# Optimization experiments

Measured on AMD Instinct MI355X. Metric: run time of the kernel, lower is better.

## Reference

```python
import jax, jax.numpy as jnp
import numpy as np

G = 320      # padded linear-hash grid extent (256 + margin for kernel offsets)
SHIFT = 16   # shift so offset coords stay non-negative


def _lin(c):
    cs = c.astype(np.int64) + SHIFT
    return (cs[:, 0] * G + cs[:, 1]) * G + cs[:, 2]


def _build_kmap(coords_in, coords_out, s):
    """Kernel map [27, N_out]: index into coords_in for each 3^3 offset (stride s), -1 if absent."""
    keys = _lin(coords_in)
    order = np.argsort(keys)
    sk = keys[order]
    offs = np.array([[i, j, k] for i in (-s, 0, s) for j in (-s, 0, s) for k in (-s, 0, s)], np.int64)
    kmap = np.full((27, coords_out.shape[0]), -1, np.int64)
    for t in range(27):
        q = _lin(coords_out + offs[t])
        pos = np.clip(np.searchsorted(sk, q), 0, sk.shape[0] - 1)
        m = sk[pos] == q
        kmap[t] = np.where(m, order[pos], -1)
    return kmap


def _downsample(coords, ns):
    return np.unique((coords // ns) * ns, axis=0)


def setup_inputs() -> dict:
    rng = np.random.default_rng(0)
    coords0 = np.unique(rng.integers(0, 256, size=(320000, 3), dtype=np.int64), axis=0)
    coords1 = _downsample(coords0, 2)
    coords2 = _downsample(coords1, 4)
    coords3 = _downsample(coords2, 8)

    km0 = _build_kmap(coords0, coords0, 1)   # conv0, ts=1
    kmd0 = _build_kmap(coords0, coords1, 1)  # down0 -> ts=2
    km1 = _build_kmap(coords1, coords1, 2)   # conv1, ts=2
    kmd1 = _build_kmap(coords1, coords2, 2)  # down1 -> ts=4
    km2 = _build_kmap(coords2, coords2, 4)   # conv2, ts=4
    kmd2 = _build_kmap(coords2, coords3, 4)  # down2 -> ts=8

    key = jax.random.key(0)
    ks = jax.random.split(key, 13)
    p = lambda k, shp: jax.random.normal(k, shp, jnp.float32) * 0.05
    return {
        "x": jax.random.normal(ks[0], (coords0.shape[0], 3), jnp.float32),
        "km0": jnp.asarray(km0), "kmd0": jnp.asarray(kmd0),
        "km1": jnp.asarray(km1), "kmd1": jnp.asarray(kmd1),
        "km2": jnp.asarray(km2), "kmd2": jnp.asarray(kmd2),
        "W0": p(ks[1], (27, 3, 64)), "b0": p(ks[2], (64,)),
        "Wd0": p(ks[3], (27, 64, 128)), "bd0": p(ks[4], (128,)),
        "W1": p(ks[5], (27, 128, 128)), "b1": p(ks[6], (128,)),
        "Wd1": p(ks[7], (27, 128, 128)), "bd1": p(ks[8], (128,)),
        "W2": p(ks[9], (27, 128, 128)), "b2": p(ks[10], (128,)),
        "Wd2": p(ks[11], (27, 128, 128)), "bd2": p(ks[12], (128,)),
    }


def _sconv(f, kmap, W, b):
    # gather-GEMM-scatter sparse conv: out[n] = b + sum_k f[kmap[k,n]] @ W[k]
    N = kmap.shape[1]
    out = jnp.zeros((N, W.shape[2]), f.dtype) + b
    for k in range(27):  # fixed small kernel loop
        idx = kmap[k]
        g = jnp.where(idx[:, None] >= 0, f[jnp.clip(idx, 0)], 0.0)
        out = out + g @ W[k]
    return out


def reference(x, km0, kmd0, km1, kmd1, km2, kmd2,
              W0, b0, Wd0, bd0, W1, b1, Wd1, bd1, W2, b2, Wd2, bd2):
    h = _sconv(x, km0, W0, b0)
    out0 = jax.nn.relu(_sconv(h, kmd0, Wd0, bd0))
    h = _sconv(out0, km1, W1, b1)
    out1 = jax.nn.relu(_sconv(h, kmd1, Wd1, bd1))
    h = _sconv(out1, km2, W2, b2)
    out2 = _sconv(h, kmd2, Wd2, bd2)  # no relu on the last output (matches torch forward)
    return (out2, out1, out0)
```

## Files before the change

### kernel.cpp

```cpp
#include <hip/hip_runtime.h>
#include <stdint.h>

typedef __bf16 bf16x8 __attribute__((ext_vector_type(8)));
typedef float f32x4 __attribute__((ext_vector_type(4)));

__device__ __forceinline__ uint32_t f2bf(float f) {
  uint32_t u = __builtin_bit_cast(uint32_t, f);
  return (u + 0x7fffu + ((u >> 16) & 1u)) >> 16;
}

__device__ __forceinline__ void gld_lds16(const void* g, void* l) {
  __builtin_amdgcn_global_load_lds(
      (const __attribute__((address_space(1))) void*)g,
      (__attribute__((address_space(3))) void*)l, 16, 0, 0);
}

__global__ void wprep_kernel(const float* __restrict__ W, uint16_t* __restrict__ Wt, int Cin) {
  int total = 27 * Cin * 128;
  for (int i = blockIdx.x * blockDim.x + threadIdx.x; i < total; i += gridDim.x * blockDim.x) {
    int k  = i / (Cin * 128);
    int r  = i - k * Cin * 128;
    int co = r / Cin;
    int ci = r - co * Cin;
    Wt[i] = (uint16_t)f2bf(W[(k * Cin + ci) * 128 + co]);
  }
}

__global__ __launch_bounds__(256) void conv0_kernel(
    const float* __restrict__ x, const int* __restrict__ km,
    const float* __restrict__ W0, const float* __restrict__ b0,
    uint16_t* __restrict__ h0, int N) {
  __shared__ float Ws[27 * 192 + 64];
  for (int i = threadIdx.x; i < 27 * 192; i += 256) Ws[i] = W0[i];
  if (threadIdx.x < 64) Ws[27 * 192 + threadIdx.x] = b0[threadIdx.x];
  __syncthreads();
  const int n = blockIdx.x * 256 + threadIdx.x;
  if (n >= N) return;

  int idx[27];
  #pragma unroll
  for (int k = 0; k < 27; ++k) idx[k] = km[(size_t)k * N + n];

  f32x4 acc[16];
  #pragma unroll
  for (int c = 0; c < 16; ++c) acc[c] = *(const f32x4*)&Ws[27 * 192 + c * 4];

  #pragma unroll
  for (int k = 0; k < 27; ++k) {
    if (idx[k] >= 0) {
      const float* xr = x + (size_t)idx[k] * 3;
      const float x0 = xr[0], x1 = xr[1], x2 = xr[2];
      const float* wk = Ws + k * 192;
      #pragma unroll
      for (int c = 0; c < 16; ++c) {
        const f32x4 w0 = *(const f32x4*)(wk + c * 4);
        const f32x4 w1 = *(const f32x4*)(wk + 64 + c * 4);
        const f32x4 w2 = *(const f32x4*)(wk + 128 + c * 4);
        acc[c] += x0 * w0 + x1 * w1 + x2 * w2;
      }
    }
  }

  uint16_t* out = h0 + (size_t)n * 64;
  #pragma unroll
  for (int g = 0; g < 8; ++g) {
    int4 v;
    v.x = (int)(f2bf(acc[g * 2][0]) | (f2bf(acc[g * 2][1]) << 16));
    v.y = (int)(f2bf(acc[g * 2][2]) | (f2bf(acc[g * 2][3]) << 16));
    v.z = (int)(f2bf(acc[g * 2 + 1][0]) | (f2bf(acc[g * 2 + 1][1]) << 16));
    v.w = (int)(f2bf(acc[g * 2 + 1][2]) | (f2bf(acc[g * 2 + 1][3]) << 16));
    *(int4*)(out + g * 8) = v;
  }
}

template <int CIN, bool OUTF32, bool RELU, bool SHADOW>
__global__ __launch_bounds__(512, 4) void sconv_pipe2_kernel(
    const uint16_t* __restrict__ fin, const int* __restrict__ kmap,
    const uint16_t* __restrict__ Wt, const float* __restrict__ bias,
    float* __restrict__ outf, uint16_t* __restrict__ outb,
    const uint16_t* __restrict__ zp, int Nout) {
  constexpr int QH = CIN / 32;
  constexpr int S = 27 * QH;
  __shared__ __align__(16) uint16_t As[2][256 * 32];
  __shared__ __align__(16) uint16_t Bs[2][128 * 32];
  __shared__ int idxs[27 * 256];

  const int t = threadIdx.x;
  const int lane = t & 63, w = t >> 6;
  const int wr = w >> 1, wc = w & 1;

  const int nwg = gridDim.x;
  int bid = blockIdx.x;
  if (nwg >= 8) {
    const int q = nwg >> 3, r = nwg & 7;
    const int xcd = bid & 7, pos = bid >> 3;
    bid = (xcd < r ? xcd * (q + 1) : r * (q + 1) + (xcd - r) * q) + pos;
  }
  const int n0 = bid * 256;

  for (int i = t; i < 27 * 256; i += 512) {
    int n = n0 + (i & 255);
    idxs[i] = (n < Nout) ? kmap[(size_t)(i >> 8) * Nout + n] : -1;
  }
  __syncthreads();

  f32x4 acc[4][4] = {};

  auto stage = [&](int ss, int nb) {
    const int k = ss / QH;
    const int q = ss % QH;
    #pragma unroll
    for (int j = 0; j < 2; ++j) {
      const int base = w * 64 + j * 512;
      const int row = (base >> 2) + (lane >> 2);
      const int sw = (lane & 3) ^ ((row >> 1) & 3);
      const int idx = idxs[k * 256 + row];
      const void* srcA = (idx >= 0)
          ? (const void*)(fin + (size_t)idx * CIN + q * 32 + sw * 8)
          : (const void*)zp;
      gld_lds16(srcA, (char*)&As[nb][0] + base * 16);
    }
    {
      const uint16_t* wk = Wt + (size_t)k * 128 * CIN + q * 32;
      const int row = t >> 2;
      const int sw = (t & 3) ^ ((row >> 1) & 3);
      gld_lds16((const void*)(wk + (size_t)row * CIN + sw * 8),
                (char*)&Bs[nb][0] + (w * 64) * 16);
    }
  };

  stage(0, 0);
  __syncthreads();

  int cur = 0;
  for (int s = 0; s < S; ++s) {
    if (s + 1 < S) stage(s + 1, cur ^ 1);
    const char* Ab = (const char*)&As[cur][0];
    const char* Bb = (const char*)&Bs[cur][0];
    bf16x8 a[4], b[4];
    const int cl = lane >> 4;
    #pragma unroll
    for (int m = 0; m < 4; ++m) {
      int row = wr * 64 + m * 16 + (lane & 15);
      a[m] = *(const bf16x8*)(Ab + row * 64 + ((cl ^ ((row >> 1) & 3)) * 16));
    }
    #pragma unroll
    for (int n = 0; n < 4; ++n) {
      int row = wc * 64 + n * 16 + (lane & 15);
      b[n] = *(const bf16x8*)(Bb + row * 64 + ((cl ^ ((row >> 1) & 3)) * 16));
    }
    #pragma unroll
    for (int m = 0; m < 4; ++m)
      #pragma unroll
      for (int n = 0; n < 4; ++n)
        acc[m][n] = __builtin_amdgcn_mfma_f32_16x16x32_bf16(a[m], b[n], acc[m][n], 0, 0, 0);
    __syncthreads();
    cur ^= 1;
  }

  #pragma unroll
  for (int m = 0; m < 4; ++m) {
    int rbase = n0 + wr * 64 + m * 16 + ((lane >> 4) << 2);
    #pragma unroll
    for (int r = 0; r < 4; ++r) {
      int gr = rbase + r;
      if (gr < Nout) {
        #pragma unroll
        for (int n = 0; n < 4; ++n) {
          int col = wc * 64 + n * 16 + (lane & 15);
          float v = acc[m][n][r] + bias[col];
          if (RELU) v = fmaxf(v, 0.f);
          if (OUTF32) outf[(size_t)gr * 128 + col] = v;
          if (SHADOW) outb[(size_t)gr * 128 + col] = (uint16_t)f2bf(v);
        }
      }
    }
  }
}

template <int CIN, bool IN_F32, bool RELU, bool WF32>
__global__ __launch_bounds__(256) void sconv_mfma_kernel(
    const void* __restrict__ fin, const int* __restrict__ kmap,
    const uint16_t* __restrict__ Wt, const float* __restrict__ bias,
    void* __restrict__ outp, int Nout) {
  constexpr int ROWB = CIN * 2;
  constexpr int CHR  = CIN / 8;
  constexpr int CPT  = (128 * CHR) / 256;
  __shared__ __align__(16) uint16_t As[128 * CIN];
  __shared__ __align__(16) uint16_t Bs[128 * CIN];
  const int t = threadIdx.x;
  const int lane = t & 63, w = t >> 6;
  const int wr = w >> 1, wc = w & 1;
  const int n0 = blockIdx.x * 128;
  f32x4 acc[4][4] = {};
  for (int k = 0; k < 27; ++k) {
    const int* __restrict__ km = kmap + (size_t)k * Nout;
    #pragma unroll
    for (int j = 0; j < CPT; ++j) {
      int c = t + j * 256;
      int row = c / CHR, c16 = c - row * CHR;
      int n = n0 + row;
      int idx = (n < Nout) ? km[n] : -1;
      int4 v = {0, 0, 0, 0};
      if (idx >= 0) {
        if (IN_F32) {
          const float* src = (const float*)fin + (size_t)idx * CIN + c16 * 8;
          float4 lo = *(const float4*)src;
          float4 hi = *(const float4*)(src + 4);
          v.x = (int)(f2bf(lo.x) | (f2bf(lo.y) << 16));
          v.y = (int)(f2bf(lo.z) | (f2bf(lo.w) << 16));
          v.z = (int)(f2bf(hi.x) | (f2bf(hi.y) << 16));
          v.w = (int)(f2bf(hi.z) | (f2bf(hi.w) << 16));
        } else {
          v = *(const int4*)((const uint16_t*)fin + (size_t)idx * CIN + c16 * 8);
        }
      }
      *(int4*)((char*)As + row * ROWB + ((c16 * 16) ^ ((row & 7) << 4))) = v;
    }
    const uint16_t* __restrict__ wkp = Wt + (size_t)k * 128 * CIN;
    #pragma unroll
    for (int j = 0; j < CPT; ++j) {
      int c = t + j * 256;
      int row = c / CHR, c16 = c - row * CHR;
      int4 v = *(const int4*)(wkp + row * CIN + c16 * 8);
      *(int4*)((char*)Bs + row * ROWB + ((c16 * 16) ^ ((row & 7) << 4))) = v;
    }
    __syncthreads();
    #pragma unroll
    for (int kk = 0; kk < CIN / 32; ++kk) {
      const int kb = (kk * 32 + ((lane >> 4) * 8)) * 2;
      bf16x8 a[4], b[4];
      #pragma unroll
      for (int m = 0; m < 4; ++m) {
        int row = wr * 64 + m * 16 + (lane & 15);
        a[m] = *(const bf16x8*)((const char*)As + row * ROWB + (kb ^ ((row & 7) << 4)));
      }
      #pragma unroll
      for (int n = 0; n < 4; ++n) {
        int row = wc * 64 + n * 16 + (lane & 15);
        b[n] = *(const bf16x8*)((const char*)Bs + row * ROWB + (kb ^ ((row & 7) << 4)));
      }
      #pragma unroll
      for (int m = 0; m < 4; ++m)
        #pragma unroll
        for (int n = 0; n < 4; ++n)
          acc[m][n] = __builtin_amdgcn_mfma_f32_16x16x32_bf16(a[m], b[n], acc[m][n], 0, 0, 0);
    }
    __syncthreads();
  }
  #pragma unroll
  for (int m = 0; m < 4; ++m) {
    int rbase = n0 + wr * 64 + m * 16 + ((lane >> 4) << 2);
    #pragma unroll
    for (int r = 0; r < 4; ++r) {
      int gr = rbase + r;
      if (gr < Nout) {
        #pragma unroll
        for (int n = 0; n < 4; ++n) {
          int col = wc * 64 + n * 16 + (lane & 15);
          float v = acc[m][n][r] + bias[col];
          if (RELU) v = fmaxf(v, 0.f);
          if (WF32) ((float*)outp)[(size_t)gr * 128 + col] = v;
          else      ((uint16_t*)outp)[(size_t)gr * 128 + col] = (uint16_t)f2bf(v);
        }
      }
    }
  }
}

extern "C" void kernel_launch(void* const* d_in, const int* in_sizes, int n_in,
                              void* d_out, int out_size, void* d_ws, size_t ws_size,
                              hipStream_t stream) {
  const float* x    = (const float*)d_in[0];
  const int*   km0  = (const int*)d_in[1];
  const int*   kmd0 = (const int*)d_in[2];
  const int*   km1  = (const int*)d_in[3];
  const int*   kmd1 = (const int*)d_in[4];
  const int*   km2  = (const int*)d_in[5];
  const int*   kmd2 = (const int*)d_in[6];
  const float* W0   = (const float*)d_in[7];
  const float* b0   = (const float*)d_in[8];
  const float* Wd0  = (const float*)d_in[9];
  const float* bd0  = (const float*)d_in[10];
  const float* W1   = (const float*)d_in[11];
  const float* b1   = (const float*)d_in[12];
  const float* Wd1  = (const float*)d_in[13];
  const float* bd1  = (const float*)d_in[14];
  const float* W2   = (const float*)d_in[15];
  const float* b2   = (const float*)d_in[16];
  const float* Wd2  = (const float*)d_in[17];
  const float* bd2  = (const float*)d_in[18];

  const int N0 = in_sizes[1] / 27;
  const int N1 = in_sizes[2] / 27;
  const int N2 = in_sizes[4] / 27;
  const int N3 = in_sizes[6] / 27;

  float* out2 = (float*)d_out;
  float* out1 = out2 + (size_t)N3 * 128;
  float* out0 = out1 + (size_t)N2 * 128;

  const size_t wsz_d0 = (size_t)27 * 64 * 128 * 2;
  const size_t wsz    = (size_t)27 * 128 * 128 * 2;
  const size_t bufA_b = 2 * ((size_t)N0 * 64 > (size_t)N1 * 128 ? (size_t)N0 * 64 : (size_t)N1 * 128);
  const size_t bufB_b = 2 * (size_t)((N1 > N2 ? N1 : N2)) * 128;

  char* p = (char*)d_ws;
  uint16_t* zp    = (uint16_t*)p; p += 512;
  uint16_t* Wt_d0 = (uint16_t*)p; p += wsz_d0;
  uint16_t* Wt_1  = (uint16_t*)p; p += wsz;
  uint16_t* Wt_d1 = (uint16_t*)p; p += wsz;
  uint16_t* Wt_2  = (uint16_t*)p; p += wsz;
  uint16_t* Wt_d2 = (uint16_t*)p; p += wsz;
  uint16_t* bufA  = (uint16_t*)p; p += bufA_b;
  uint16_t* bufB  = (uint16_t*)p;

  const size_t needed_new = 512 + wsz_d0 + 4 * wsz + bufA_b + bufB_b;

  wprep_kernel<<<dim3((27 * 64 * 128 + 255) / 256), dim3(256), 0, stream>>>(Wd0, Wt_d0, 64);
  wprep_kernel<<<dim3((27 * 128 * 128 + 255) / 256), dim3(256), 0, stream>>>(W1, Wt_1, 128);
  wprep_kernel<<<dim3((27 * 128 * 128 + 255) / 256), dim3(256), 0, stream>>>(Wd1, Wt_d1, 128);
  wprep_kernel<<<dim3((27 * 128 * 128 + 255) / 256), dim3(256), 0, stream>>>(W2, Wt_2, 128);
  wprep_kernel<<<dim3((27 * 128 * 128 + 255) / 256), dim3(256), 0, stream>>>(Wd2, Wt_d2, 128);

  if (ws_size >= needed_new) {
    hipMemsetAsync(zp, 0, 512, stream);
    conv0_kernel<<<dim3((N0 + 255) / 256), dim3(256), 0, stream>>>(x, km0, W0, b0, bufA, N0);
    sconv_pipe2_kernel<64, true, true, true>
        <<<dim3((N1 + 255) / 256), dim3(512), 0, stream>>>(bufA, kmd0, Wt_d0, bd0, out0, bufB, zp, N1);
    sconv_pipe2_kernel<128, false, false, true>
        <<<dim3((N1 + 255) / 256), dim3(512), 0, stream>>>(bufB, km1, Wt_1, b1, nullptr, bufA, zp, N1);
    sconv_pipe2_kernel<128, true, true, true>
        <<<dim3((N2 + 255) / 256), dim3(512), 0, stream>>>(bufA, kmd1, Wt_d1, bd1, out1, bufB, zp, N2);
    sconv_pipe2_kernel<128, false, false, true>
        <<<dim3((N2 + 255) / 256), dim3(512), 0, stream>>>(bufB, km2, Wt_2, b2, nullptr, bufA, zp, N2);
    sconv_pipe2_kernel<128, true, false, false>
        <<<dim3((N3 + 255) / 256), dim3(512), 0, stream>>>(bufA, kmd2, Wt_d2, bd2, out2, nullptr, zp, N3);
  } else {
    uint16_t* hbuf = (uint16_t*)((char*)d_ws + 512 + wsz_d0 + 4 * wsz);
    conv0_kernel<<<dim3((N0 + 255) / 256), dim3(256), 0, stream>>>(x, km0, W0, b0, hbuf, N0);
    sconv_mfma_kernel<64, false, true, true>
        <<<dim3((N1 + 127) / 128), dim3(256), 0, stream>>>(hbuf, kmd0, Wt_d0, bd0, out0, N1);
    sconv_mfma_kernel<128, true, false, false>
        <<<dim3((N1 + 127) / 128), dim3(256), 0, stream>>>(out0, km1, Wt_1, b1, hbuf, N1);
    sconv_mfma_kernel<128, false, true, true>
        <<<dim3((N2 + 127) / 128), dim3(256), 0, stream>>>(hbuf, kmd1, Wt_d1, bd1, out1, N2);
    sconv_mfma_kernel<128, true, false, false>
        <<<dim3((N2 + 127) / 128), dim3(256), 0, stream>>>(out1, km2, Wt_2, b2, hbuf, N2);
    sconv_mfma_kernel<128, false, false, true>
        <<<dim3((N3 + 127) / 128), dim3(256), 0, stream>>>(hbuf, kmd2, Wt_d2, bd2, out2, N3);
  }
}
```

Before: 1.032 ms.

## Triple-buffer LDS staging with explicit vmcnt waits and single barrier per step

Turns the two-buffer gather/weight staging in the sparse-conv MFMA kernel into a three-buffer pipeline that keeps two stages of async global-to-LDS loads in flight. Each step waits on vmcnt for the oldest stage, then issues one barrier before launching the next load, which removes the trailing __syncthreads. This aims to hide gather latency better. In exchange it uses more LDS and lowers the occupancy hint from 4 to 2 waves per SIMD, and it depends on the per-thread load count matching vmcnt(3).

```diff
diff --git a/kernel.cpp b/kernel.cpp
--- a/kernel.cpp
+++ b/kernel.cpp
@@ -74,15 +74,15 @@
 }
 
 template <int CIN, bool OUTF32, bool RELU, bool SHADOW>
-__global__ __launch_bounds__(512, 4) void sconv_pipe2_kernel(
+__global__ __launch_bounds__(512, 2) void sconv_pipe3_kernel(
     const uint16_t* __restrict__ fin, const int* __restrict__ kmap,
     const uint16_t* __restrict__ Wt, const float* __restrict__ bias,
     float* __restrict__ outf, uint16_t* __restrict__ outb,
     const uint16_t* __restrict__ zp, int Nout) {
   constexpr int QH = CIN / 32;
   constexpr int S = 27 * QH;
-  __shared__ __align__(16) uint16_t As[2][256 * 32];
-  __shared__ __align__(16) uint16_t Bs[2][128 * 32];
+  __shared__ __align__(16) uint16_t As[3][256 * 32];
+  __shared__ __align__(16) uint16_t Bs[3][128 * 32];
   __shared__ int idxs[27 * 256];
 
   const int t = threadIdx.x;
@@ -106,9 +106,10 @@
 
   f32x4 acc[4][4] = {};
 
-  auto stage = [&](int ss, int nb) {
+  auto stage = [&](int ss) {
+    const int nb = ss % 3;
     const int k = ss / QH;
-    const int q = ss % QH;
+    const int q = ss & (QH - 1);
     #pragma unroll
     for (int j = 0; j < 2; ++j) {
       const int base = w * 64 + j * 512;
@@ -129,14 +130,19 @@
     }
   };
 
-  stage(0, 0);
-  __syncthreads();
-
-  int cur = 0;
+  stage(0);
+  stage(1);
+
   for (int s = 0; s < S; ++s) {
-    if (s + 1 < S) stage(s + 1, cur ^ 1);
-    const char* Ab = (const char*)&As[cur][0];
-    const char* Bb = (const char*)&Bs[cur][0];
+    if (s + 1 < S) asm volatile("s_waitcnt vmcnt(3)" ::: "memory");
+    else           asm volatile("s_waitcnt vmcnt(0)" ::: "memory");
+    __builtin_amdgcn_sched_barrier(0);
+    __builtin_amdgcn_s_barrier();
+    __builtin_amdgcn_sched_barrier(0);
+    if (s + 2 < S) stage(s + 2);
+
+    const char* Ab = (const char*)&As[s % 3][0];
+    const char* Bb = (const char*)&Bs[s % 3][0];
     bf16x8 a[4], b[4];
     const int cl = lane >> 4;
     #pragma unroll
@@ -154,8 +160,6 @@
       #pragma unroll
       for (int n = 0; n < 4; ++n)
         acc[m][n] = __builtin_amdgcn_mfma_f32_16x16x32_bf16(a[m], b[n], acc[m][n], 0, 0, 0);
-    __syncthreads();
-    cur ^= 1;
   }
 
   #pragma unroll
@@ -326,15 +330,15 @@
   if (ws_size >= needed_new) {
     hipMemsetAsync(zp, 0, 512, stream);
     conv0_kernel<<<dim3((N0 + 255) / 256), dim3(256), 0, stream>>>(x, km0, W0, b0, bufA, N0);
-    sconv_pipe2_kernel<64, true, true, true>
+    sconv_pipe3_kernel<64, true, true, true>
         <<<dim3((N1 + 255) / 256), dim3(512), 0, stream>>>(bufA, kmd0, Wt_d0, bd0, out0, bufB, zp, N1);
-    sconv_pipe2_kernel<128, false, false, true>
+    sconv_pipe3_kernel<128, false, false, true>
         <<<dim3((N1 + 255) / 256), dim3(512), 0, stream>>>(bufB, km1, Wt_1, b1, nullptr, bufA, zp, N1);
-    sconv_pipe2_kernel<128, true, true, true>
+    sconv_pipe3_kernel<128, true, true, true>
         <<<dim3((N2 + 255) / 256), dim3(512), 0, stream>>>(bufA, kmd1, Wt_d1, bd1, out1, bufB, zp, N2);
-    sconv_pipe2_kernel<128, false, false, true>
+    sconv_pipe3_kernel<128, false, false, true>
         <<<dim3((N2 + 255) / 256), dim3(512), 0, stream>>>(bufB, km2, Wt_2, b2, nullptr, bufA, zp, N2);
-    sconv_pipe2_kernel<128, true, false, false>
+    sconv_pipe3_kernel<128, true, false, false>
         <<<dim3((N3 + 255) / 256), dim3(512), 0, stream>>>(bufA, kmd2, Wt_d2, bd2, out2, nullptr, zp, N3);
   } else {
     uint16_t* hbuf = (uint16_t*)((char*)d_ws + 512 + wsz_d0 + 4 * wsz);
```

New measurement: 1.460 ms. 1.41x slower.
